# Kernel optimization log

Measured on AMD Instinct MI355X. Metric: run time of the kernel, lower is better.

Reference implementation:

```python
import jax, jax.numpy as jnp
import numpy as np

N, K, D = 1_048_576, 16, 8
EPS = 1e-6


def setup_inputs() -> dict:
    key = jax.random.key(0)
    k1, k2, k3, k4 = jax.random.split(key, 4)
    x = jax.random.normal(k1, (N, D), dtype=jnp.float32)
    means = jax.random.normal(k2, (K, D), dtype=jnp.float32)
    # near-identity Cholesky factors so L @ L.T is well conditioned
    chol_var = jnp.broadcast_to(jnp.eye(D, dtype=jnp.float32), (K, D, D)) \
        + 0.05 * jax.random.normal(k3, (K, D, D), dtype=jnp.float32)
    pi = jnp.ones((K,), dtype=jnp.float32) / K \
        + 0.1 * jax.random.uniform(k4, (K,), dtype=jnp.float32)
    return {"x": x, "means": means, "chol_var": chol_var, "pi": pi}


def reference(x, means, chol_var, pi):
    d = x.shape[-1]
    # per-component covariance: tril(L) @ tril(L)^T + eps*I  -> [K, D, D]
    Ltri = jnp.tril(chol_var)
    cov = jnp.einsum('kij,klj->kil', Ltri, Ltri) + EPS * jnp.eye(d, dtype=x.dtype)
    # MultivariateNormal(mean, cov).log_prob == Cholesky of cov + triangular solve
    L = jnp.linalg.cholesky(cov)                                 # [K, D, D]
    diff = x[:, None, :] - means[None, :, :]                     # [N, K, D]
    b = jnp.transpose(diff, (1, 2, 0))                           # [K, D, N]
    y = jax.scipy.linalg.solve_triangular(L, b, lower=True)      # [K, D, N]
    quad = jnp.sum(y * y, axis=1)                                # [K, N]
    half_logdet = jnp.sum(jnp.log(jnp.diagonal(L, axis1=-2, axis2=-1)), axis=-1)  # [K]
    log2pi = jnp.log(jnp.asarray(2.0 * np.pi, dtype=x.dtype))
    log_probs = -0.5 * (quad + d * log2pi) - half_logdet[:, None]  # [K, N]
    # mixture weights via log_softmax, stable logsumexp over components
    weighted = log_probs.T + jax.nn.log_softmax(pi)              # [N, K]
    return jax.nn.logsumexp(weighted, axis=1)                    # [N]
```

## Files before the change

### kernel.cpp

```cpp
#include <hip/hip_runtime.h>
#include <hip/hip_bf16.h>
#include <math.h>

#define KCOMP 16
#define DDIM 8
#define CSTRIDE 48
#define PPT 8

__global__ void gmm_precompute(const float* __restrict__ means,
                               const float* __restrict__ chol_var,
                               const float* __restrict__ pi,
                               float* __restrict__ coef) {
    __shared__ float sconst[KCOMP];
    int k = threadIdx.x;
    if (k < KCOMP) {
        float Lc[DDIM][DDIM];
#pragma unroll
        for (int i = 0; i < DDIM; ++i)
#pragma unroll
            for (int j = 0; j < DDIM; ++j)
                Lc[i][j] = (j <= i) ? chol_var[k * DDIM * DDIM + i * DDIM + j] : 0.0f;

        float C[DDIM][DDIM];
#pragma unroll
        for (int i = 0; i < DDIM; ++i)
#pragma unroll
            for (int j = 0; j < DDIM; ++j) {
                if (j > i) { C[i][j] = 0.0f; continue; }
                float s = 0.0f;
#pragma unroll
                for (int m = 0; m < DDIM; ++m) s += Lc[i][m] * Lc[j][m];
                C[i][j] = s;
            }
#pragma unroll
        for (int i = 0; i < DDIM; ++i) C[i][i] += 1e-6f;

        float L[DDIM][DDIM];
#pragma unroll
        for (int i = 0; i < DDIM; ++i)
#pragma unroll
            for (int j = 0; j < DDIM; ++j) L[i][j] = 0.0f;
#pragma unroll
        for (int j = 0; j < DDIM; ++j) {
            float d = C[j][j];
#pragma unroll
            for (int m = 0; m < DDIM; ++m) if (m < j) d -= L[j][m] * L[j][m];
            float ljj = sqrtf(d);
            L[j][j] = ljj;
            float inv = 1.0f / ljj;
#pragma unroll
            for (int i = 0; i < DDIM; ++i) {
                if (i <= j) continue;
                float s = C[i][j];
#pragma unroll
                for (int m = 0; m < DDIM; ++m) if (m < j) s -= L[i][m] * L[j][m];
                L[i][j] = s * inv;
            }
        }

        float Li[DDIM][DDIM];
#pragma unroll
        for (int i = 0; i < DDIM; ++i)
#pragma unroll
            for (int j = 0; j < DDIM; ++j) Li[i][j] = 0.0f;
#pragma unroll
        for (int c = 0; c < DDIM; ++c) {
            Li[c][c] = 1.0f / L[c][c];
#pragma unroll
            for (int i = 0; i < DDIM; ++i) {
                if (i <= c) continue;
                float s = 0.0f;
#pragma unroll
                for (int m = 0; m < DDIM; ++m)
                    if (m >= c && m < i) s += L[i][m] * Li[m][c];
                Li[i][c] = -s / L[i][i];
            }
        }

        float hld = 0.0f;
#pragma unroll
        for (int i = 0; i < DDIM; ++i) hld += __logf(L[i][i]);

        float mx = pi[0];
#pragma unroll
        for (int j = 1; j < KCOMP; ++j) mx = fmaxf(mx, pi[j]);
        float ssum = 0.0f;
#pragma unroll
        for (int j = 0; j < KCOMP; ++j) ssum += __expf(pi[j] - mx);
        float lse = mx + __logf(ssum);

        const float LOG2PI = 1.83787706640934548356f;
        float constk = (pi[k] - lse) - hld - 0.5f * (float)DDIM * LOG2PI;

        const float r = 0.70710678118654752440f;
        float* c = coef + k * CSTRIDE;
        int idx = 0;
#pragma unroll
        for (int i = 0; i < DDIM; ++i)
#pragma unroll
            for (int j = 0; j < DDIM; ++j)
                if (j <= i) c[idx++] = Li[i][j] * r;
#pragma unroll
        for (int i = 0; i < DDIM; ++i) {
            float b = 0.0f;
#pragma unroll
            for (int j = 0; j < DDIM; ++j)
                if (j <= i) b += Li[i][j] * means[k * DDIM + j];
            c[36 + i] = -b * r;
        }
        c[44] = constk;
        c[45] = 0.0f; c[46] = 0.0f; c[47] = 0.0f;
        sconst[k] = constk;
    }
    __syncthreads();
    if (threadIdx.x == 0) {
        float m = sconst[0];
#pragma unroll
        for (int j = 1; j < KCOMP; ++j) m = fmaxf(m, sconst[j]);
        coef[KCOMP * CSTRIDE] = m;
    }
}

__global__ __launch_bounds__(256) void gmm_main(const float* __restrict__ x,
                                                const float* __restrict__ coef,
                                                float* __restrict__ out, int n) {
    const int base = blockIdx.x * (256 * PPT) + threadIdx.x;

    float xv[PPT][DDIM];
#pragma unroll
    for (int p = 0; p < PPT; ++p) {
        int pt = base + p * 256;
        const float4* xp = (const float4*)(x + (size_t)pt * DDIM);
        float4 a = xp[0];
        float4 b = xp[1];
        xv[p][0] = a.x; xv[p][1] = a.y; xv[p][2] = a.z; xv[p][3] = a.w;
        xv[p][4] = b.x; xv[p][5] = b.y; xv[p][6] = b.z; xv[p][7] = b.w;
    }

    const float Cmax = coef[KCOMP * CSTRIDE];
    float s[PPT];
#pragma unroll
    for (int p = 0; p < PPT; ++p) s[p] = 0.0f;

#pragma unroll 1
    for (int k = 0; k < KCOMP; ++k) {
        const float4* c4 = (const float4*)(coef + k * CSTRIDE);
        float cc[48];
#pragma unroll
        for (int t = 0; t < 12; ++t) {
            float4 v = c4[t];
            cc[4 * t + 0] = v.x; cc[4 * t + 1] = v.y;
            cc[4 * t + 2] = v.z; cc[4 * t + 3] = v.w;
        }
        const float ck = cc[44] - Cmax;
#pragma unroll
        for (int p = 0; p < PPT; ++p) {
            float q = 0.0f;
            int idx = 0;
#pragma unroll
            for (int i = 0; i < DDIM; ++i) {
                float y = cc[36 + i];
#pragma unroll
                for (int j = 0; j <= i; ++j) { y = fmaf(cc[idx], xv[p][j], y); ++idx; }
                q = fmaf(y, y, q);
            }
            s[p] += __expf(ck - q);
        }
    }

#pragma unroll
    for (int p = 0; p < PPT; ++p) {
        int pt = base + p * 256;
        if (pt < n) out[pt] = Cmax + __logf(s[p]);
    }
}

extern "C" void kernel_launch(void* const* d_in, const int* in_sizes, int n_in,
                              void* d_out, int out_size, void* d_ws, size_t ws_size,
                              hipStream_t stream) {
    const float* x        = (const float*)d_in[0];
    const float* means    = (const float*)d_in[1];
    const float* chol_var = (const float*)d_in[2];
    const float* pi       = (const float*)d_in[3];
    float* out  = (float*)d_out;
    float* coef = (float*)d_ws;

    int n = in_sizes[0] / DDIM;

    gmm_precompute<<<1, 64, 0, stream>>>(means, chol_var, pi, coef);
    int nthreads = (n + PPT - 1) / PPT;
    gmm_main<<<(nthreads + 255) / 256, 256, 0, stream>>>(x, coef, out, n);
}
```

Before: 105.4 us.

## Fuse coefficient precompute into main kernel with per-block shared-memory coefficients

```diff
diff --git a/kernel.cpp b/kernel.cpp
--- a/kernel.cpp
+++ b/kernel.cpp
@@ -7,12 +7,14 @@
 #define CSTRIDE 48
 #define PPT 8
 
-__global__ void gmm_precompute(const float* __restrict__ means,
-                               const float* __restrict__ chol_var,
-                               const float* __restrict__ pi,
-                               float* __restrict__ coef) {
-    __shared__ float sconst[KCOMP];
-    int k = threadIdx.x;
+__global__ __launch_bounds__(256) void gmm_fused(const float* __restrict__ x,
+                                                 const float* __restrict__ means,
+                                                 const float* __restrict__ chol_var,
+                                                 const float* __restrict__ pi,
+                                                 float* __restrict__ out, int n) {
+    __shared__ float sc[KCOMP * CSTRIDE];
+
+    const int k = threadIdx.x;
     if (k < KCOMP) {
         float Lc[DDIM][DDIM];
 #pragma unroll
@@ -25,8 +27,7 @@
 #pragma unroll
         for (int i = 0; i < DDIM; ++i)
 #pragma unroll
-            for (int j = 0; j < DDIM; ++j) {
-                if (j > i) { C[i][j] = 0.0f; continue; }
+            for (int j = 0; j <= i; ++j) {
                 float s = 0.0f;
 #pragma unroll
                 for (int m = 0; m < DDIM; ++m) s += Lc[i][m] * Lc[j][m];
@@ -36,10 +37,6 @@
         for (int i = 0; i < DDIM; ++i) C[i][i] += 1e-6f;
 
         float L[DDIM][DDIM];
-#pragma unroll
-        for (int i = 0; i < DDIM; ++i)
-#pragma unroll
-            for (int j = 0; j < DDIM; ++j) L[i][j] = 0.0f;
 #pragma unroll
         for (int j = 0; j < DDIM; ++j) {
             float d = C[j][j];
@@ -93,7 +90,7 @@
         float constk = (pi[k] - lse) - hld - 0.5f * (float)DDIM * LOG2PI;
 
         const float r = 0.70710678118654752440f;
-        float* c = coef + k * CSTRIDE;
+        float* c = sc + k * CSTRIDE;
         int idx = 0;
 #pragma unroll
         for (int i = 0; i < DDIM; ++i)
@@ -110,22 +107,14 @@
         }
         c[44] = constk;
         c[45] = 0.0f; c[46] = 0.0f; c[47] = 0.0f;
-        sconst[k] = constk;
     }
     __syncthreads();
-    if (threadIdx.x == 0) {
-        float m = sconst[0];
+
+    float Cmax = sc[44];
 #pragma unroll
-        for (int j = 1; j < KCOMP; ++j) m = fmaxf(m, sconst[j]);
-        coef[KCOMP * CSTRIDE] = m;
-    }
-}
+    for (int j = 1; j < KCOMP; ++j) Cmax = fmaxf(Cmax, sc[j * CSTRIDE + 44]);
 
-__global__ __launch_bounds__(256) void gmm_main(const float* __restrict__ x,
-                                                const float* __restrict__ coef,
-                                                float* __restrict__ out, int n) {
     const int base = blockIdx.x * (256 * PPT) + threadIdx.x;
-
     float xv[PPT][DDIM];
 #pragma unroll
     for (int p = 0; p < PPT; ++p) {
@@ -137,14 +126,13 @@
         xv[p][4] = b.x; xv[p][5] = b.y; xv[p][6] = b.z; xv[p][7] = b.w;
     }
 
-    const float Cmax = coef[KCOMP * CSTRIDE];
     float s[PPT];
 #pragma unroll
     for (int p = 0; p < PPT; ++p) s[p] = 0.0f;
 
 #pragma unroll 1
-    for (int k = 0; k < KCOMP; ++k) {
-        const float4* c4 = (const float4*)(coef + k * CSTRIDE);
+    for (int kk = 0; kk < KCOMP; ++kk) {
+        const float4* c4 = (const float4*)(sc + kk * CSTRIDE);
         float cc[48];
 #pragma unroll
         for (int t = 0; t < 12; ++t) {
@@ -182,12 +170,9 @@
     const float* means    = (const float*)d_in[1];
     const float* chol_var = (const float*)d_in[2];
     const float* pi       = (const float*)d_in[3];
-    float* out  = (float*)d_out;
-    float* coef = (float*)d_ws;
+    float* out = (float*)d_out;
 
     int n = in_sizes[0] / DDIM;
-
-    gmm_precompute<<<1, 64, 0, stream>>>(means, chol_var, pi, coef);
     int nthreads = (n + PPT - 1) / PPT;
-    gmm_main<<<(nthreads + 255) / 256, 256, 0, stream>>>(x, coef, out, n);
+    gmm_fused<<<(nthreads + 255) / 256, 256, 0, stream>>>(x, means, chol_var, pi, out, n);
 }
```

New measurement: 98.80 us. -6.3%, faster.
